# Kernel tuning notes

Hardware: AMD Instinct MI355X
Metric: run time of the kernel (lower is better)

Reference implementation:

```python
import jax, jax.numpy as jnp
import numpy as np

DIM = 256
HEADS = 8
HEAD_DIM = DIM // HEADS
WS = (2, 8, 8)  # window size (t, h, w)
N = WS[0] * WS[1] * WS[2]  # 128 tokens per window
SCALE = HEAD_DIM ** -0.5
MLP_HIDDEN = int(DIM * 2.0)
EPS = 1e-5

# static relative-position index table [N, N]
def _rel_pos_index():
    coords = np.stack(np.meshgrid(np.arange(WS[0]), np.arange(WS[1]), np.arange(WS[2]), indexing='ij'))
    cf = coords.reshape(3, -1)
    rel = cf[:, :, None] - cf[:, None, :]
    rel = rel.transpose(1, 2, 0).copy()
    rel[..., 0] += WS[0] - 1
    rel[..., 1] += WS[1] - 1
    rel[..., 2] += WS[2] - 1
    rel[..., 0] *= (2 * WS[1] - 1) * (2 * WS[2] - 1)
    rel[..., 1] *= (2 * WS[2] - 1)
    return rel.sum(-1)

REL_IDX = jnp.asarray(_rel_pos_index())  # [N, N] int
TABLE_SIZE = (2 * WS[0] - 1) * (2 * WS[1] - 1) * (2 * WS[2] - 1)  # 675


def layernorm(x, g, b):
    m = jnp.mean(x, axis=-1, keepdims=True)
    var = jnp.mean(jnp.square(x - m), axis=-1, keepdims=True)
    return (x - m) * jax.lax.rsqrt(var + EPS) * g + b


def window_partition(x):
    B, T, H, W, C = x.shape
    x = x.reshape(B, T // WS[0], WS[0], H // WS[1], WS[1], W // WS[2], WS[2], C)
    x = x.transpose(0, 1, 3, 5, 2, 4, 6, 7)
    return x.reshape(-1, N, C)


def window_reverse(wins, B, T, H, W):
    C = wins.shape[-1]
    x = wins.reshape(B, T // WS[0], H // WS[1], W // WS[2], WS[0], WS[1], WS[2], C)
    x = x.transpose(0, 1, 4, 2, 5, 3, 6, 7)
    return x.reshape(B, T, H, W, C)


def setup_inputs() -> dict:
    key = jax.random.key(0)
    ks = jax.random.split(key, 20)
    B, T, H, W = 2, 8, 64, 64
    f = lambda k, s, sc=0.02: jax.random.normal(k, s, dtype=jnp.float32) * sc
    return {
        'q': jax.random.normal(ks[0], (B, T, H, W, DIM), dtype=jnp.float32),
        'k': jax.random.normal(ks[1], (B, T, H, W, DIM), dtype=jnp.float32),
        'v': jax.random.normal(ks[2], (B, T, H, W, DIM), dtype=jnp.float32),
        'gq': jnp.ones((DIM,), jnp.float32), 'bq': jnp.zeros((DIM,), jnp.float32),
        'gk': jnp.ones((DIM,), jnp.float32), 'bk': jnp.zeros((DIM,), jnp.float32),
        'gv': jnp.ones((DIM,), jnp.float32), 'bv': jnp.zeros((DIM,), jnp.float32),
        'bias_table': f(ks[3], (TABLE_SIZE, HEADS)),
        'proj_w': f(ks[4], (DIM, DIM)), 'proj_b': jnp.zeros((DIM,), jnp.float32),
        'g2': jnp.ones((DIM,), jnp.float32), 'b2': jnp.zeros((DIM,), jnp.float32),
        'mw1': f(ks[5], (MLP_HIDDEN, DIM)), 'mb1': jnp.zeros((MLP_HIDDEN,), jnp.float32),
        'mw2': f(ks[6], (DIM, MLP_HIDDEN)), 'mb2': jnp.zeros((DIM,), jnp.float32),
    }


def reference(q, k, v, gq, bq, gk, bk, gv, bv, bias_table, proj_w, proj_b, g2, b2, mw1, mb1, mw2, mb2):
    B, T, H, W, C = q.shape
    shortcut = v
    qn = layernorm(q, gq, bq)
    kn = layernorm(k, gk, bk)
    vn = layernorm(v, gv, bv)
    # (dims divisible by window -> no padding needed)
    qw = window_partition(qn)  # [B_, N, C]
    kw = window_partition(kn)
    vw = window_partition(vn)
    B_ = qw.shape[0]
    to_heads = lambda t: t.reshape(B_, N, HEADS, HEAD_DIM).transpose(0, 2, 1, 3)  # [B_, h, N, d]
    qh, kh, vh = to_heads(qw), to_heads(kw), to_heads(vw)
    attn = jnp.einsum('bhnd,bhmd->bhnm', qh * SCALE, kh)
    bias = bias_table[REL_IDX]  # [N, N, heads]
    attn = attn + bias.transpose(2, 0, 1)[None]
    attn = jax.nn.softmax(attn, axis=-1)
    out = jnp.einsum('bhnm,bhmd->bhnd', attn, vh)
    out = out.transpose(0, 2, 1, 3).reshape(B_, N, C)
    out = out @ proj_w.T + proj_b
    x = window_reverse(out, B, T, H, W)
    x = shortcut + x
    h1 = layernorm(x, g2, b2)
    h1 = jax.nn.gelu(h1 @ mw1.T + mb1, approximate=False)
    x = x + (h1 @ mw2.T + mb2)
    return x
```

## Files before the change

kernel.cpp:

```cpp
#include <hip/hip_runtime.h>
#include <math.h>


typedef __attribute__((ext_vector_type(8))) short short8;
typedef __attribute__((ext_vector_type(4))) short shortx4;
typedef __attribute__((ext_vector_type(4))) float floatx4;

#define MFMA16(a, b, c) __builtin_amdgcn_mfma_f32_16x16x32_bf16((a), (b), (c), 0, 0, 0)
#define ATT_SCALE 0.17677669529663689f

__device__ __forceinline__ short f2bf(float f) {
  unsigned u = __float_as_uint(f);
  u += 0x7fffu + ((u >> 16) & 1u);
  return (short)(u >> 16);
}
__device__ __forceinline__ float bf2f(short s) {
  return __uint_as_float(((unsigned)(unsigned short)s) << 16);
}
__device__ __forceinline__ void gl2lds(const short* g, short* l) {
  __builtin_amdgcn_global_load_lds((const __attribute__((address_space(1))) void*)(g),
                                   (__attribute__((address_space(3))) void*)(l), 16, 0, 0);
}

__global__ void cvt_kernel(const float* __restrict__ src, short* __restrict__ dst, int n) {
  int i = blockIdx.x * 256 + threadIdx.x;
  if (i < n) dst[i] = f2bf(src[i]);
}

__global__ void biasprep_kernel(const float* __restrict__ table, short* __restrict__ biasPb) {
  int idx = blockIdx.x * 256 + threadIdx.x;
  int h = idx >> 14;
  int n = (idx >> 7) & 127;
  int lr = (idx >> 3) & 15;
  int c = idx & 7;
  int m = 16 * c + lr;
  int t1 = n >> 6, h1 = (n >> 3) & 7, w1 = n & 7;
  int t2 = m >> 6, h2 = (m >> 3) & 7, w2 = m & 7;
  int ridx = (t1 - t2 + 1) * 225 + (h1 - h2 + 7) * 15 + (w1 - w2 + 7);
  biasPb[idx] = f2bf(table[ridx * 8 + h]);
}

__global__ __launch_bounds__(256) void ln_qkv_kernel(
    const float* __restrict__ q, const float* __restrict__ k, const float* __restrict__ v,
    const float* __restrict__ gq, const float* __restrict__ bq,
    const float* __restrict__ gk, const float* __restrict__ bk,
    const float* __restrict__ gv, const float* __restrict__ bv,
    short* __restrict__ qw, short* __restrict__ kw, short* __restrict__ vw) {
  const int wv = threadIdx.x >> 6, l = threadIdx.x & 63;
  const int tok = blockIdx.x * 4 + wv;
  const int which = blockIdx.y;
  const float* src = (which == 0) ? q : ((which == 1) ? k : v);
  const float* gg  = (which == 0) ? gq : ((which == 1) ? gk : gv);
  const float* bb  = (which == 0) ? bq : ((which == 1) ? bk : bv);
  short* dst       = (which == 0) ? qw : ((which == 1) ? kw : vw);

  float4 xv = *(const float4*)(src + (size_t)tok * 256 + l * 4);
  float s1 = xv.x + xv.y + xv.z + xv.w;
  float s2 = xv.x * xv.x + xv.y * xv.y + xv.z * xv.z + xv.w * xv.w;
#pragma unroll
  for (int off = 1; off < 64; off <<= 1) {
    s1 += __shfl_xor(s1, off);
    s2 += __shfl_xor(s2, off);
  }
  float mean = s1 * (1.0f / 256.0f);
  float var = s2 * (1.0f / 256.0f) - mean * mean;
  float inv = rsqrtf(var + 1e-5f);

  int b_ = tok >> 15, rem = tok & 32767;
  int t = rem >> 12, hh = (rem >> 6) & 63, ww = rem & 63;
  int wi = ((b_ * 4 + (t >> 1)) * 8 + (hh >> 3)) * 8 + (ww >> 3);
  int n = ((t & 1) << 6) | ((hh & 7) << 3) | (ww & 7);

  float4 g4 = *(const float4*)(gg + l * 4);
  float4 b4 = *(const float4*)(bb + l * 4);
  shortx4 o;
  o[0] = f2bf((xv.x - mean) * inv * g4.x + b4.x);
  o[1] = f2bf((xv.y - mean) * inv * g4.y + b4.y);
  o[2] = f2bf((xv.z - mean) * inv * g4.z + b4.z);
  o[3] = f2bf((xv.w - mean) * inv * g4.w + b4.w);
  *(shortx4*)(dst + ((size_t)wi * 128 + n) * 256 + l * 4) = o;
}

__global__ __launch_bounds__(256, 4) void attn_kernel(
    const short* __restrict__ qw, const short* __restrict__ kw, const short* __restrict__ vw,
    const short* __restrict__ biasPb, short* __restrict__ ao) {
  __shared__ union SU {
    struct { short Qs[128][40]; short Ks[128][40]; } qk;
    short Ps[128 * 128];
  } su;
  __shared__ short Vt[32 * 128];

  const int wi = blockIdx.x, h = blockIdx.y, tid = threadIdx.x;
  const size_t base = (size_t)wi * 128 * 256 + h * 32;

#pragma unroll
  for (int i = 0; i < 2; ++i) {
    int idx = tid + 256 * i;
    int m = idx >> 2, c = idx & 3;
    *(short8*)&su.qk.Qs[m][c * 8] = *(const short8*)(qw + base + (size_t)m * 256 + c * 8);
    *(short8*)&su.qk.Ks[m][c * 8] = *(const short8*)(kw + base + (size_t)m * 256 + c * 8);
    short8 vv = *(const short8*)(vw + base + (size_t)m * 256 + c * 8);
#pragma unroll
    for (int e = 0; e < 8; ++e) {
      int d = c * 8 + e;
      Vt[d * 128 + (((m >> 3) ^ (d & 7)) << 3) + (m & 7)] = vv[e];
    }
  }
  __syncthreads();

  const int wvv = tid >> 6, l = tid & 63, lr = l & 15, g = l >> 4;
  const floatx4 zf = {0.f, 0.f, 0.f, 0.f};

  short8 aq0 = *(const short8*)&su.qk.Qs[32 * wvv + lr][g * 8];
  short8 aq1 = *(const short8*)&su.qk.Qs[32 * wvv + 16 + lr][g * 8];

  floatx4 s[2][8];
#pragma unroll
  for (int c = 0; c < 8; ++c) {
    short8 bk8 = *(const short8*)&su.qk.Ks[16 * c + lr][g * 8];
    s[0][c] = MFMA16(aq0, bk8, zf);
    s[1][c] = MFMA16(aq1, bk8, zf);
  }
  __syncthreads();

  const int lr7 = lr & 7;
#pragma unroll
  for (int r = 0; r < 2; ++r) {
#pragma unroll
    for (int j = 0; j < 4; ++j) {
      int n = 32 * wvv + 16 * r + 4 * g + j;
      short8 bv8 = *(const short8*)(biasPb + ((size_t)(h * 128 + n) * 16 + lr) * 8);
      float mx = -1e30f;
#pragma unroll
      for (int c = 0; c < 8; ++c) {
        float val = s[r][c][j] * ATT_SCALE + bf2f(bv8[c]);
        s[r][c][j] = val;
        mx = fmaxf(mx, val);
      }
#pragma unroll
      for (int off = 1; off < 16; off <<= 1) mx = fmaxf(mx, __shfl_xor(mx, off));
      float sum = 0.f;
#pragma unroll
      for (int c = 0; c < 8; ++c) {
        float e = __expf(s[r][c][j] - mx);
        s[r][c][j] = e;
        sum += e;
      }
#pragma unroll
      for (int off = 1; off < 16; off <<= 1) sum += __shfl_xor(sum, off);
      float invs = 1.0f / sum;
      int n7 = n & 7;
#pragma unroll
      for (int c = 0; c < 8; ++c) {
        int col = 16 * c + lr;
        su.Ps[n * 128 + (((col >> 3) ^ n7) << 3) + (col & 7)] = f2bf(s[r][c][j] * invs);
      }
    }
  }

  floatx4 o00 = zf, o01 = zf, o10 = zf, o11 = zf;
  const int ra0 = 32 * wvv + lr, ra1 = ra0 + 16;
#pragma unroll
  for (int ks = 0; ks < 4; ++ks) {
    int ulog = ks * 4 + g;
    short8 pa0 = *(const short8*)&su.Ps[ra0 * 128 + ((ulog ^ (ra0 & 7)) << 3)];
    short8 pa1 = *(const short8*)&su.Ps[ra1 * 128 + ((ulog ^ (ra1 & 7)) << 3)];
    short8 vb0 = *(const short8*)&Vt[lr * 128 + ((ulog ^ lr7) << 3)];
    short8 vb1 = *(const short8*)&Vt[(16 + lr) * 128 + ((ulog ^ lr7) << 3)];
    o00 = MFMA16(pa0, vb0, o00);
    o01 = MFMA16(pa0, vb1, o01);
    o10 = MFMA16(pa1, vb0, o10);
    o11 = MFMA16(pa1, vb1, o11);
  }
#pragma unroll
  for (int j = 0; j < 4; ++j) {
    int n0 = 32 * wvv + 4 * g + j;
    int n1 = n0 + 16;
    size_t rb0 = ((size_t)wi * 128 + n0) * 256 + h * 32;
    size_t rb1 = ((size_t)wi * 128 + n1) * 256 + h * 32;
    ao[rb0 + lr] = f2bf(o00[j]);
    ao[rb0 + 16 + lr] = f2bf(o01[j]);
    ao[rb1 + lr] = f2bf(o10[j]);
    ao[rb1 + 16 + lr] = f2bf(o11[j]);
  }
}

__global__ __launch_bounds__(256, 2) void xpath_kernel(
    const short* __restrict__ ao, const short* __restrict__ wp,
    const float* __restrict__ proj_b, const float* __restrict__ vin,
    const float* __restrict__ g2, const float* __restrict__ b2,
    const short* __restrict__ w1, const float* __restrict__ mb1,
    const short* __restrict__ w2, const float* __restrict__ mb2,
    float* __restrict__ out) {
  __shared__ short Ws[256 * 64];
  __shared__ short XL[64 * 256];
  __shared__ short H1[64 * 128];
  short* As = H1;

  const int tid = threadIdx.x;
  const int w = tid >> 6, l = tid & 63, lr = l & 15, g = l >> 4;
  const int li = l >> 3, u = l & 7;
  const int swz = ((u ^ li) << 3);
  const int s0 = ((g ^ (lr & 7)) << 3);
  const int s1 = (((4 + g) ^ (lr & 7)) << 3);
  const floatx4 zf = {0.f, 0.f, 0.f, 0.f};
  const int bx = blockIdx.x;
  const int r16 = 16 * w + lr;

  floatx4 acc1[16];
#pragma unroll
  for (int i = 0; i < 16; ++i) acc1[i] = zf;
  const short* A = ao + (size_t)bx * 64 * 256;
  for (int k0 = 0; k0 < 256; k0 += 64) {
    if (k0) __syncthreads();
#pragma unroll
    for (int c = 0; c < 2; ++c)
      gl2lds(A + (size_t)((w + 4 * c) * 8 + li) * 256 + k0 + swz, As + (w + 4 * c) * 512);
#pragma unroll
    for (int c = 0; c < 8; ++c)
      gl2lds(wp + (size_t)((w + 4 * c) * 8 + li) * 256 + k0 + swz, Ws + (w + 4 * c) * 512);
    __syncthreads();
    short8 a0 = *(const short8*)&As[r16 * 64 + s0];
    short8 a1 = *(const short8*)&As[r16 * 64 + s1];
#pragma unroll
    for (int ct = 0; ct < 16; ++ct) {
      int rb = ct * 16 + lr;
      short8 b0 = *(const short8*)&Ws[rb * 64 + s0];
      acc1[ct] = MFMA16(a0, b0, acc1[ct]);
      short8 b1 = *(const short8*)&Ws[rb * 64 + s1];
      acc1[ct] = MFMA16(a1, b1, acc1[ct]);
    }
  }

  int sidx4[4];
  float xr[16][4];
  {
    const int wiw = bx >> 1;
    const int wb = wiw & 7, hb = (wiw >> 3) & 7, tt = (wiw >> 6) & 3, b_ = wiw >> 8;
#pragma unroll
    for (int j = 0; j < 4; ++j) {
      int row = 16 * w + 4 * g + j;
      int n = ((bx & 1) << 6) | row;
      int t = tt * 2 + (n >> 6), hh = hb * 8 + ((n >> 3) & 7), ww2 = wb * 8 + (n & 7);
      int sidx = ((b_ * 8 + t) * 64 + hh) * 64 + ww2;
      sidx4[j] = sidx;
      float ss1 = 0.f, ss2 = 0.f;
#pragma unroll
      for (int ct = 0; ct < 16; ++ct) {
        int col = ct * 16 + lr;
        float val = acc1[ct][j] + proj_b[col] + vin[(size_t)sidx * 256 + col];
        xr[ct][j] = val;
        ss1 += val;
        ss2 += val * val;
      }
#pragma unroll
      for (int off = 1; off < 16; off <<= 1) {
        ss1 += __shfl_xor(ss1, off);
        ss2 += __shfl_xor(ss2, off);
      }
      float mean = ss1 * (1.0f / 256.0f);
      float var = ss2 * (1.0f / 256.0f) - mean * mean;
      float inv = rsqrtf(var + 1e-5f);
      int r7 = row & 7;
#pragma unroll
      for (int ct = 0; ct < 16; ++ct) {
        int col = ct * 16 + lr;
        float xl = (xr[ct][j] - mean) * inv * g2[col] + b2[col];
        int uu = col >> 3;
        XL[row * 256 + (((uu & 24) | ((uu & 7) ^ r7)) << 3) + (col & 7)] = f2bf(xl);
      }
    }
  }
  __syncthreads();

  floatx4 acc3[16];
#pragma unroll
  for (int i = 0; i < 16; ++i) acc3[i] = zf;

  for (int qt = 0; qt < 4; ++qt) {
    floatx4 acc2[8];
#pragma unroll
    for (int i = 0; i < 8; ++i) acc2[i] = zf;
    for (int k0 = 0; k0 < 256; k0 += 64) {
      __syncthreads();
#pragma unroll
      for (int c = 0; c < 4; ++c)
        gl2lds(w1 + (size_t)(qt * 128 + (w + 4 * c) * 8 + li) * 256 + k0 + swz,
               Ws + (w + 4 * c) * 512);
      __syncthreads();
      short8 a0 = *(const short8*)&XL[r16 * 256 + k0 + ((g ^ (r16 & 7)) << 3)];
      short8 a1 = *(const short8*)&XL[r16 * 256 + k0 + (((4 + g) ^ (r16 & 7)) << 3)];
#pragma unroll
      for (int ct = 0; ct < 8; ++ct) {
        int rb = ct * 16 + lr;
        short8 b0 = *(const short8*)&Ws[rb * 64 + s0];
        acc2[ct] = MFMA16(a0, b0, acc2[ct]);
        short8 b1 = *(const short8*)&Ws[rb * 64 + s1];
        acc2[ct] = MFMA16(a1, b1, acc2[ct]);
      }
    }
#pragma unroll
    for (int ct = 0; ct < 8; ++ct) {
      int col = ct * 16 + lr;
      float bias = mb1[qt * 128 + col];
#pragma unroll
      for (int j = 0; j < 4; ++j) {
        int row = 16 * w + 4 * g + j;
        float val = acc2[ct][j] + bias;
        float ge = 0.5f * val * (1.0f + erff(val * 0.70710678118654752f));
        int uu = col >> 3;
        H1[row * 128 + (((uu & 8) | ((uu & 7) ^ (row & 7))) << 3) + (col & 7)] = f2bf(ge);
      }
    }
    for (int k0 = 0; k0 < 128; k0 += 64) {
      __syncthreads();
#pragma unroll
      for (int c = 0; c < 8; ++c)
        gl2lds(w2 + (size_t)((w + 4 * c) * 8 + li) * 512 + qt * 128 + k0 + swz,
               Ws + (w + 4 * c) * 512);
      __syncthreads();
      short8 a0 = *(const short8*)&H1[r16 * 128 + k0 + ((g ^ (r16 & 7)) << 3)];
      short8 a1 = *(const short8*)&H1[r16 * 128 + k0 + (((4 + g) ^ (r16 & 7)) << 3)];
#pragma unroll
      for (int ct = 0; ct < 16; ++ct) {
        int rb = ct * 16 + lr;
        short8 b0 = *(const short8*)&Ws[rb * 64 + s0];
        acc3[ct] = MFMA16(a0, b0, acc3[ct]);
        short8 b1 = *(const short8*)&Ws[rb * 64 + s1];
        acc3[ct] = MFMA16(a1, b1, acc3[ct]);
      }
    }
  }

#pragma unroll
  for (int ct = 0; ct < 16; ++ct) {
    int col = ct * 16 + lr;
    float bias = mb2[col];
#pragma unroll
    for (int j = 0; j < 4; ++j)
      out[(size_t)sidx4[j] * 256 + col] = xr[ct][j] + acc3[ct][j] + bias;
  }
}

extern "C" void kernel_launch(void* const* d_in, const int* in_sizes, int n_in,
                              void* d_out, int out_size, void* d_ws, size_t ws_size,
                              hipStream_t stream) {
  const float* q = (const float*)d_in[0];
  const float* k = (const float*)d_in[1];
  const float* v = (const float*)d_in[2];
  const float* gq = (const float*)d_in[3];
  const float* bq = (const float*)d_in[4];
  const float* gk = (const float*)d_in[5];
  const float* bk = (const float*)d_in[6];
  const float* gv = (const float*)d_in[7];
  const float* bv = (const float*)d_in[8];
  const float* bias_table = (const float*)d_in[9];
  const float* proj_w = (const float*)d_in[10];
  const float* proj_b = (const float*)d_in[11];
  const float* g2 = (const float*)d_in[12];
  const float* b2 = (const float*)d_in[13];
  const float* mw1 = (const float*)d_in[14];
  const float* mb1 = (const float*)d_in[15];
  const float* mw2 = (const float*)d_in[16];
  const float* mb2 = (const float*)d_in[17];

  char* ws = (char*)d_ws;
  short* qw = (short*)(ws + 0);
  short* kw = (short*)(ws + 33554432);
  short* vw = (short*)(ws + 67108864);
  short* ao = (short*)(ws + 100663296);
  short* wp = (short*)(ws + 167772160);
  short* w1 = (short*)(ws + 167903232);
  short* w2 = (short*)(ws + 168165376);
  short* biasPb = (short*)(ws + 168427520);

  cvt_kernel<<<256, 256, 0, stream>>>(proj_w, wp, 65536);
  cvt_kernel<<<512, 256, 0, stream>>>(mw1, w1, 131072);
  cvt_kernel<<<512, 256, 0, stream>>>(mw2, w2, 131072);
  biasprep_kernel<<<512, 256, 0, stream>>>(bias_table, biasPb);

  ln_qkv_kernel<<<dim3(16384, 3), 256, 0, stream>>>(q, k, v, gq, bq, gk, bk, gv, bv, qw, kw, vw);

  attn_kernel<<<dim3(512, 8), 256, 0, stream>>>(qw, kw, vw, biasPb, ao);

  xpath_kernel<<<1024, 256, 0, stream>>>(ao, wp, proj_b, v, g2, b2, w1, mb1, w2, mb2,
                                         (float*)d_out);
}
```

Before: 236.8 us.

## Process 128-row tiles with 512-thread blocks in fused projection/MLP kernel

The fused projection+LayerNorm+MLP kernel now handles a full 128-token window per block with 8 wavefronts instead of 64 rows with 4, so each weight tile staged in LDS is reused across twice as many rows. The A operand of the projection GEMM is loaded directly from global memory into registers instead of being staged through LDS, and the barrier after the LayerNorm stage is dropped. The cost is fewer, larger blocks with more LDS (about 128KB), which allows one block per CU and may lower latency hiding. The unswizzled direct A loads may also be less coalesced than the old LDS path.

```diff
diff --git a/kernel.cpp b/kernel.cpp
--- a/kernel.cpp
+++ b/kernel.cpp
@@ -185,7 +185,7 @@
   }
 }
 
-__global__ __launch_bounds__(256, 2) void xpath_kernel(
+__global__ __launch_bounds__(512, 1) void xpath_kernel(
     const short* __restrict__ ao, const short* __restrict__ wp,
     const float* __restrict__ proj_b, const float* __restrict__ vin,
     const float* __restrict__ g2, const float* __restrict__ b2,
@@ -193,9 +193,8 @@
     const short* __restrict__ w2, const float* __restrict__ mb2,
     float* __restrict__ out) {
   __shared__ short Ws[256 * 64];
-  __shared__ short XL[64 * 256];
-  __shared__ short H1[64 * 128];
-  short* As = H1;
+  __shared__ short XL[128 * 256];
+  __shared__ short H1[128 * 128];
 
   const int tid = threadIdx.x;
   const int w = tid >> 6, l = tid & 63, lr = l & 15, g = l >> 4;
@@ -206,22 +205,21 @@
   const floatx4 zf = {0.f, 0.f, 0.f, 0.f};
   const int bx = blockIdx.x;
   const int r16 = 16 * w + lr;
+  const size_t grow = (size_t)bx * 128;
 
   floatx4 acc1[16];
 #pragma unroll
   for (int i = 0; i < 16; ++i) acc1[i] = zf;
-  const short* A = ao + (size_t)bx * 64 * 256;
   for (int k0 = 0; k0 < 256; k0 += 64) {
-    if (k0) __syncthreads();
-#pragma unroll
-    for (int c = 0; c < 2; ++c)
-      gl2lds(A + (size_t)((w + 4 * c) * 8 + li) * 256 + k0 + swz, As + (w + 4 * c) * 512);
-#pragma unroll
-    for (int c = 0; c < 8; ++c)
-      gl2lds(wp + (size_t)((w + 4 * c) * 8 + li) * 256 + k0 + swz, Ws + (w + 4 * c) * 512);
+    short8 a0 = *(const short8*)(ao + (grow + r16) * 256 + k0 + g * 8);
+    short8 a1 = *(const short8*)(ao + (grow + r16) * 256 + k0 + 32 + g * 8);
     __syncthreads();
-    short8 a0 = *(const short8*)&As[r16 * 64 + s0];
-    short8 a1 = *(const short8*)&As[r16 * 64 + s1];
+#pragma unroll
+    for (int i = 0; i < 4; ++i) {
+      int c = w + 8 * i;
+      gl2lds(wp + (size_t)(8 * c + li) * 256 + k0 + swz, Ws + c * 512);
+    }
+    __syncthreads();
 #pragma unroll
     for (int ct = 0; ct < 16; ++ct) {
       int rb = ct * 16 + lr;
@@ -235,13 +233,11 @@
   int sidx4[4];
   float xr[16][4];
   {
-    const int wiw = bx >> 1;
-    const int wb = wiw & 7, hb = (wiw >> 3) & 7, tt = (wiw >> 6) & 3, b_ = wiw >> 8;
+    const int wb = bx & 7, hb = (bx >> 3) & 7, tt = (bx >> 6) & 3, b_ = bx >> 8;
 #pragma unroll
     for (int j = 0; j < 4; ++j) {
       int row = 16 * w + 4 * g + j;
-      int n = ((bx & 1) << 6) | row;
-      int t = tt * 2 + (n >> 6), hh = hb * 8 + ((n >> 3) & 7), ww2 = wb * 8 + (n & 7);
+      int t = tt * 2 + (row >> 6), hh = hb * 8 + ((row >> 3) & 7), ww2 = wb * 8 + (row & 7);
       int sidx = ((b_ * 8 + t) * 64 + hh) * 64 + ww2;
       sidx4[j] = sidx;
       float ss1 = 0.f, ss2 = 0.f;
@@ -271,7 +267,6 @@
       }
     }
   }
-  __syncthreads();
 
   floatx4 acc3[16];
 #pragma unroll
@@ -284,9 +279,10 @@
     for (int k0 = 0; k0 < 256; k0 += 64) {
       __syncthreads();
 #pragma unroll
-      for (int c = 0; c < 4; ++c)
-        gl2lds(w1 + (size_t)(qt * 128 + (w + 4 * c) * 8 + li) * 256 + k0 + swz,
-               Ws + (w + 4 * c) * 512);
+      for (int i = 0; i < 2; ++i) {
+        int c = w + 8 * i;
+        gl2lds(w1 + (size_t)(qt * 128 + 8 * c + li) * 256 + k0 + swz, Ws + c * 512);
+      }
       __syncthreads();
       short8 a0 = *(const short8*)&XL[r16 * 256 + k0 + ((g ^ (r16 & 7)) << 3)];
       short8 a1 = *(const short8*)&XL[r16 * 256 + k0 + (((4 + g) ^ (r16 & 7)) << 3)];
@@ -315,9 +311,10 @@
     for (int k0 = 0; k0 < 128; k0 += 64) {
       __syncthreads();
 #pragma unroll
-      for (int c = 0; c < 8; ++c)
-        gl2lds(w2 + (size_t)((w + 4 * c) * 8 + li) * 512 + qt * 128 + k0 + swz,
-               Ws + (w + 4 * c) * 512);
+      for (int i = 0; i < 4; ++i) {
+        int c = w + 8 * i;
+        gl2lds(w2 + (size_t)(8 * c + li) * 512 + qt * 128 + k0 + swz, Ws + c * 512);
+      }
       __syncthreads();
       short8 a0 = *(const short8*)&H1[r16 * 128 + k0 + ((g ^ (r16 & 7)) << 3)];
       short8 a1 = *(const short8*)&H1[r16 * 128 + k0 + (((4 + g) ^ (r16 & 7)) << 3)];
@@ -383,6 +380,6 @@
 
   attn_kernel<<<dim3(512, 8), 256, 0, stream>>>(qw, kw, vw, biasPb, ao);
 
-  xpath_kernel<<<1024, 256, 0, stream>>>(ao, wp, proj_b, v, g2, b2, w1, mb1, w2, mb2,
-                                         (float*)d_out);
-}
+  xpath_kernel<<<512, 512, 0, stream>>>(ao, wp, proj_b, v, g2, b2, w1, mb1, w2, mb2,
+                                        (float*)d_out);
+}
```

After: 225.8 us. 1.05x faster.
